# Optimization experiments

Measured on AMD Instinct MI355X. Metric: run time of the kernel, lower is better.

## Reference

```python
import jax, jax.numpy as jnp
import numpy as np

TEMPERATURE = 0.1
TIME_THRESHOLD = 365
NEG = -1e9  # stands in for -inf; exp(NEG - max) == 0 exactly in fp32
EPS = 1e-12  # F.normalize eps


def setup_inputs() -> dict:
    key = jax.random.key(0)
    k1, k2, k3 = jax.random.split(key, 3)
    B, D = 8192, 128
    embeddings = jax.random.normal(k1, (B, D), dtype=jnp.float32)
    survival_times = jax.random.randint(k2, (B,), 0, 3650, dtype=jnp.int32)
    censor = jax.random.randint(k3, (B,), 0, 2, dtype=jnp.int32)
    return {"embeddings": embeddings, "survival_times": survival_times, "censor": censor}


def reference(embeddings, survival_times, censor):
    B = embeddings.shape[0]
    # L2 normalize rows (torch F.normalize semantics)
    norm = jnp.maximum(jnp.linalg.norm(embeddings, axis=1, keepdims=True), EPS)
    z = embeddings / norm
    # pairwise cosine similarity / temperature: [B, B]
    sim = jnp.einsum('ik,jk->ij', z, z) / TEMPERATURE
    diag = jnp.eye(B, dtype=bool)
    sim = jnp.where(diag, NEG, sim)  # mask self-similarity
    # positive mask: |t_i - t_j| < threshold, i != j, row i uncensored
    tdiff = jnp.abs(survival_times[:, None] - survival_times[None, :])
    pos = (tdiff < TIME_THRESHOLD) & (~diag) & (censor[:, None] == 1)
    # per-row masked logsumexp reductions
    denominator = jax.nn.logsumexp(sim, axis=1)                      # [B]
    numerator = jax.nn.logsumexp(jnp.where(pos, sim, NEG), axis=1)   # [B]
    has_pos = jnp.any(pos, axis=1)
    per_row = jnp.where(has_pos, denominator - numerator, 0.0)
    cnt = jnp.sum(has_pos.astype(jnp.float32))
    return jnp.where(cnt > 0, jnp.sum(per_row) / jnp.maximum(cnt, 1.0), 0.0)
```

## Files before the change

kernel.cpp:

```cpp
#include <hip/hip_runtime.h>
#include <cstdint>

#define BDIM 8192
#define DDIM 128
#define JS 32

#define ZH_OFF 0
#define ZL_OFF (2 * 1024 * 1024)
#define RL_OFF (4 * 1024 * 1024)
#define CNT_OFF (RL_OFF + BDIM * 4)
#define FC_OFF (CNT_OFF + 64)
#define P_OFF (RL_OFF + 65536)
#define PART_OFF (P_OFF + BDIM * JS * 8)

typedef __attribute__((ext_vector_type(8))) short bf16x8;
typedef __attribute__((ext_vector_type(4))) float f32x4;

__device__ __forceinline__ short f2bf(float f) {
  unsigned u = __float_as_uint(f);
  unsigned r = (u + 0x7fffu + ((u >> 16) & 1u)) >> 16;
  return (short)r;
}
__device__ __forceinline__ float bf2f(short h) {
  return __uint_as_float(((unsigned)(unsigned short)h) << 16);
}
__device__ __forceinline__ void gload_lds16(const void* g, void* l) {
  __builtin_amdgcn_global_load_lds(
      (const __attribute__((address_space(1))) unsigned int*)g,
      (__attribute__((address_space(3))) unsigned int*)l, 16, 0, 0);
}


__global__ __launch_bounds__(256) void ck_prep(
    const float* __restrict__ emb, const int* __restrict__ censor,
    short* __restrict__ ZhT, short* __restrict__ ZlT,
    int* __restrict__ rowlist, int* __restrict__ cnt, int* __restrict__ fc)
{
  __shared__ float zl[16][132];
  __shared__ float pr[16][16];
  __shared__ float inv[16];
  __shared__ int wtot[4], woff[4];

  const int t = threadIdx.x;
  if (blockIdx.x == 512) {
    const int lane = t & 63, wv = t >> 6;
    const int4* c4 = (const int4*)(censor + t * 32);
    unsigned fm = 0;
#pragma unroll
    for (int q = 0; q < 8; ++q) {
      const int4 v = c4[q];
      fm |= (unsigned)(v.x == 1) << (q * 4 + 0);
      fm |= (unsigned)(v.y == 1) << (q * 4 + 1);
      fm |= (unsigned)(v.z == 1) << (q * 4 + 2);
      fm |= (unsigned)(v.w == 1) << (q * 4 + 3);
    }
    const int loc = __popc(fm);
    int sc = loc;
#pragma unroll
    for (int m = 1; m < 64; m <<= 1) {
      const int u = __shfl_up(sc, m, 64);
      if (lane >= m) sc += u;
    }
    if (lane == 63) wtot[wv] = sc;
    __syncthreads();
    if (t == 0) {
      int run = 0;
#pragma unroll
      for (int i = 0; i < 4; ++i) { woff[i] = run; run += wtot[i]; }
      fc[0] = 0;
    }
    __syncthreads();
    int off = woff[wv] + sc - loc;
    for (int u = 0; u < 32; ++u)
      if ((fm >> u) & 1) rowlist[off++] = t * 32 + u;
    if (t == 255) cnt[0] = off;
    return;
  }

  const int R = blockIdx.x;
  const int r16 = t >> 4, seg = t & 15;
  const float4* src = (const float4*)(emb + (size_t)(R * 16 + r16) * DDIM + seg * 8);
  const float4 v0 = src[0], v1 = src[1];
  float* zr = &zl[r16][seg * 8];
  zr[0] = v0.x; zr[1] = v0.y; zr[2] = v0.z; zr[3] = v0.w;
  zr[4] = v1.x; zr[5] = v1.y; zr[6] = v1.z; zr[7] = v1.w;
  pr[r16][seg] = v0.x * v0.x + v0.y * v0.y + v0.z * v0.z + v0.w * v0.w +
                 v1.x * v1.x + v1.y * v1.y + v1.z * v1.z + v1.w * v1.w;
  __syncthreads();
  if (t < 16) {
    float ss = 0.f;
#pragma unroll
    for (int s = 0; s < 16; ++s) ss += pr[t][s];
    inv[t] = 1.0f / fmaxf(sqrtf(ss), 1e-12f);
  }
  __syncthreads();
  const int kc = t >> 6, hf = (t >> 4) & 3, rw = t & 15;
  const float iv = inv[rw];
  const float* zs = &zl[rw][(kc * 4 + hf) * 8];
  short hs[8], ls[8];
#pragma unroll
  for (int j = 0; j < 8; ++j) {
    const float z = zs[j] * iv;
    const short h = f2bf(z);
    hs[j] = h;
    ls[j] = f2bf(z - bf2f(h));
  }
  const int dst = R * 2048 + t * 8;
  *(bf16x8*)(ZhT + dst) = *(const bf16x8*)hs;
  *(bf16x8*)(ZlT + dst) = *(const bf16x8*)ls;
}

__global__ __launch_bounds__(256, 2) void ck_main(
    const short* __restrict__ ZhT, const short* __restrict__ ZlT,
    const int* __restrict__ rowlist, const int* __restrict__ cntp,
    const int* __restrict__ times, float2* __restrict__ P2)
{
  __shared__ __align__(16) char lds[65536];
  const int cnt = *cntp;
  const int t = threadIdx.x;
  const int b = blockIdx.x;
  const int lane = t & 63;
  const int w = t >> 6;
  const int half = lane >> 4;
  const int ll = lane & 15;
  const int js = b & 31;
  const int jR0 = js * 16;

  for (int g = b >> 5; g * 256 < cnt; g += 16) {
    int rbase[4];
#pragma unroll
    for (int a = 0; a < 4; ++a) {
      int c = g * 256 + w * 64 + a * 16 + ll;
      if (c >= cnt) c = cnt - 1;
      const int r = rowlist[c];
      rbase[a] = (r >> 4) * 2048 + (r & 15) * 8;
    }
    bf16x8 ah[4][4];
#pragma unroll
    for (int a = 0; a < 4; ++a)
#pragma unroll
      for (int kc = 0; kc < 4; ++kc)
        ah[a][kc] = *(const bf16x8*)(ZhT + rbase[a] + kc * 512 + half * 128);

    int meta[4][4];
#pragma unroll
    for (int a = 0; a < 4; ++a)
#pragma unroll
      for (int r = 0; r < 4; ++r) {
        const int idx = g * 256 + w * 64 + a * 16 + half * 4 + r;
        const bool vi = idx < cnt;
        const int gi = rowlist[vi ? idx : 0];
        const int taP = vi ? (times[gi] + 364) : 50000;
        meta[a][r] = (taP << 16) | (vi ? gi : 0xFFFF);
      }

    float sd[4][4] = {{0.f}}, sn[4][4] = {{0.f}};

    {
      const int c0 = w * 8;
#pragma unroll
      for (int u = 0; u < 8; ++u) {
        const int c = c0 + u, cp = c & 15;
        const short* src = (c < 16) ? ZhT : ZlT;
        const short* gp = src + (size_t)(jR0 + (cp >> 2)) * 2048 + (cp & 3) * 512 + lane * 8;
        gload_lds16(gp, lds + ((c < 16) ? 0 : 16384) + cp * 1024);
      }
    }

    for (int st = 0; st < 4; ++st) {
      __syncthreads();
      if (st < 3) {
        const int pB = ((st + 1) & 1) * 32768;
        const int c0 = w * 8;
#pragma unroll
        for (int u = 0; u < 8; ++u) {
          const int c = c0 + u, cp = c & 15;
          const short* src = (c < 16) ? ZhT : ZlT;
          const short* gp = src + (size_t)(jR0 + (st + 1) * 4 + (cp >> 2)) * 2048 + (cp & 3) * 512 + lane * 8;
          gload_lds16(gp, lds + pB + ((c < 16) ? 0 : 16384) + cp * 1024);
        }
      }

      const char* L = lds + (st & 1) * 32768;
      f32x4 acc[4][4];
#pragma unroll
      for (int a = 0; a < 4; ++a)
#pragma unroll
        for (int bb = 0; bb < 4; ++bb) acc[a][bb] = (f32x4){0.f, 0.f, 0.f, 0.f};

#pragma unroll
      for (int kc = 0; kc < 4; ++kc) {
        bf16x8 bh[4], bl[4];
#pragma unroll
        for (int bb = 0; bb < 4; ++bb) {
          bh[bb] = *(const bf16x8*)(L + bb * 4096 + kc * 1024 + lane * 16);
          bl[bb] = *(const bf16x8*)(L + 16384 + bb * 4096 + kc * 1024 + lane * 16);
        }
#pragma unroll
        for (int a = 0; a < 4; ++a)
#pragma unroll
          for (int bb = 0; bb < 4; ++bb)
            acc[a][bb] = __builtin_amdgcn_mfma_f32_16x16x32_bf16(ah[a][kc], bh[bb], acc[a][bb], 0, 0, 0);
#pragma unroll
        for (int a = 0; a < 4; ++a)
#pragma unroll
          for (int bb = 0; bb < 4; ++bb)
            acc[a][bb] = __builtin_amdgcn_mfma_f32_16x16x32_bf16(ah[a][kc], bl[bb], acc[a][bb], 0, 0, 0);
#pragma unroll
        for (int a = 0; a < 4; ++a) {
          const bf16x8 alv = *(const bf16x8*)(ZlT + rbase[a] + kc * 512 + half * 128);
#pragma unroll
          for (int bb = 0; bb < 4; ++bb)
            acc[a][bb] = __builtin_amdgcn_mfma_f32_16x16x32_bf16(alv, bh[bb], acc[a][bb], 0, 0, 0);
        }
      }

      const int jb = js * 256 + st * 64;
      int tJ[4];
#pragma unroll
      for (int bb = 0; bb < 4; ++bb) tJ[bb] = times[jb + bb * 16 + ll];
#pragma unroll
      for (int a = 0; a < 4; ++a)
#pragma unroll
        for (int r = 0; r < 4; ++r) {
          const int m_ = meta[a][r];
          const int gi = m_ & 0xFFFF;
          const unsigned taP = ((unsigned)m_) >> 16;
          float d = 0.f, n = 0.f;
#pragma unroll
          for (int bb = 0; bb < 4; ++bb) {
            const int jgb = jb + bb * 16 + ll;
            float pv = __expf(fmaf(acc[a][bb][r], 10.f, -10.f));
            pv = (gi == jgb) ? 0.f : pv;
            d += pv;
            n += ((unsigned)(taP - (unsigned)tJ[bb]) <= 728u) ? pv : 0.f;
          }
          sd[a][r] += d;
          sn[a][r] += n;
        }
    }

#pragma unroll
    for (int a = 0; a < 4; ++a)
#pragma unroll
      for (int r = 0; r < 4; ++r) {
        float d = sd[a][r], n = sn[a][r];
#pragma unroll
        for (int m = 1; m <= 8; m <<= 1) {
          d += __shfl_xor(d, m, 64);
          n += __shfl_xor(n, m, 64);
        }
        const int idx = g * 256 + w * 64 + a * 16 + half * 4 + r;
        if (ll == 0 && idx < cnt) P2[(size_t)idx * JS + js] = make_float2(d, n);
      }
    __syncthreads();
  }
}

__global__ __launch_bounds__(256) void ck_fin(
    const float2* __restrict__ P2, const int* __restrict__ cntp,
    float2* __restrict__ part, int* __restrict__ fc, float* __restrict__ out)
{
  const int cnt = *cntp;
  const int t = threadIdx.x;
  const int idx = blockIdx.x * 256 + t;
  float lsum = 0.f, lcnt = 0.f;
  if (idx < cnt) {
    const float4* p = (const float4*)(P2 + (size_t)idx * JS);
    float d = 0.f, n = 0.f;
#pragma unroll
    for (int u = 0; u < 16; ++u) {
      const float4 v = p[u];
      d += v.x + v.z;
      n += v.y + v.w;
    }
    if (n > 0.f) { lsum = logf(d) - logf(n); lcnt = 1.f; }
  }
  __shared__ float s1[256], s2[256];
  __shared__ int amLast;
  s1[t] = lsum; s2[t] = lcnt;
  __syncthreads();
  for (int s = 128; s > 0; s >>= 1) {
    if (t < s) { s1[t] += s1[t + s]; s2[t] += s2[t + s]; }
    __syncthreads();
  }
  if (t == 0) {
    part[blockIdx.x] = make_float2(s1[0], s2[0]);
    __threadfence();
    amLast = (atomicAdd(fc, 1) == gridDim.x - 1);
  }
  __syncthreads();
  if (amLast) {
    __threadfence();
    float s = 0.f, c = 0.f;
    if (t < 32) { const float2 v = part[t]; s = v.x; c = v.y; }
    if (t < 64) {
#pragma unroll
      for (int m = 1; m < 64; m <<= 1) {
        s += __shfl_xor(s, m, 64);
        c += __shfl_xor(c, m, 64);
      }
      if (t == 0) out[0] = (c > 0.f) ? s / fmaxf(c, 1.f) : 0.f;
    }
  }
}

extern "C" void kernel_launch(void* const* d_in, const int* in_sizes, int n_in,
                              void* d_out, int out_size, void* d_ws, size_t ws_size,
                              hipStream_t stream) {
  const float* emb  = (const float*)d_in[0];
  const int* times  = (const int*)d_in[1];
  const int* censor = (const int*)d_in[2];
  float* out = (float*)d_out;

  char* ws = (char*)d_ws;
  short* ZhT    = (short*)(ws + ZH_OFF);
  short* ZlT    = (short*)(ws + ZL_OFF);
  int* rowlist  = (int*)(ws + RL_OFF);
  int* cntp     = (int*)(ws + CNT_OFF);
  int* fc       = (int*)(ws + FC_OFF);
  float2* P2    = (float2*)(ws + P_OFF);
  float2* part  = (float2*)(ws + PART_OFF);

  ck_prep<<<513, 256, 0, stream>>>(emb, censor, ZhT, ZlT, rowlist, cntp, fc);
  ck_main<<<512, 256, 0, stream>>>(ZhT, ZlT, rowlist, cntp, times, P2);
  ck_fin<<<32, 256, 0, stream>>>(P2, cntp, part, fc, out);
}
```

Baseline: 131.9 us.

## Replace persistent row-group loop with one 128-row tile per block

The main kernel no longer loops over 256-row groups inside 512 persistent blocks. It now launches 2048 blocks, each handling one 128-row tile (two 16-row subtiles per wave) and exiting early when past the uncensored row count. The MFMA loop is reordered so each B fragment is loaded from LDS once and used immediately for the hi/lo products, which cuts register pressure from 16 accumulators to 8. This aims for better occupancy and load balance. The cost is that each block reloads the full column strip into LDS for fewer rows, so each column tile is reused less.

```diff
diff --git a/kernel.cpp b/kernel.cpp
--- a/kernel.cpp
+++ b/kernel.cpp
@@ -119,142 +119,133 @@
   const int cnt = *cntp;
   const int t = threadIdx.x;
   const int b = blockIdx.x;
+  const int it = b >> 5;
+  const int js = b & 31;
+  if (it * 128 >= cnt) return;
   const int lane = t & 63;
   const int w = t >> 6;
   const int half = lane >> 4;
   const int ll = lane & 15;
-  const int js = b & 31;
   const int jR0 = js * 16;
 
-  for (int g = b >> 5; g * 256 < cnt; g += 16) {
-    int rbase[4];
-#pragma unroll
-    for (int a = 0; a < 4; ++a) {
-      int c = g * 256 + w * 64 + a * 16 + ll;
-      if (c >= cnt) c = cnt - 1;
-      const int r = rowlist[c];
-      rbase[a] = (r >> 4) * 2048 + (r & 15) * 8;
-    }
-    bf16x8 ah[4][4];
-#pragma unroll
-    for (int a = 0; a < 4; ++a)
-#pragma unroll
-      for (int kc = 0; kc < 4; ++kc)
-        ah[a][kc] = *(const bf16x8*)(ZhT + rbase[a] + kc * 512 + half * 128);
-
-    int meta[4][4];
-#pragma unroll
-    for (int a = 0; a < 4; ++a)
-#pragma unroll
-      for (int r = 0; r < 4; ++r) {
-        const int idx = g * 256 + w * 64 + a * 16 + half * 4 + r;
-        const bool vi = idx < cnt;
-        const int gi = rowlist[vi ? idx : 0];
-        const int taP = vi ? (times[gi] + 364) : 50000;
-        meta[a][r] = (taP << 16) | (vi ? gi : 0xFFFF);
-      }
-
-    float sd[4][4] = {{0.f}}, sn[4][4] = {{0.f}};
-
-    {
+  int rbase[2];
+#pragma unroll
+  for (int a = 0; a < 2; ++a) {
+    int c = it * 128 + w * 32 + a * 16 + ll;
+    if (c >= cnt) c = cnt - 1;
+    const int r = rowlist[c];
+    rbase[a] = (r >> 4) * 2048 + (r & 15) * 8;
+  }
+  bf16x8 ah[2][4];
+#pragma unroll
+  for (int a = 0; a < 2; ++a)
+#pragma unroll
+    for (int kc = 0; kc < 4; ++kc)
+      ah[a][kc] = *(const bf16x8*)(ZhT + rbase[a] + kc * 512 + half * 128);
+
+  int meta[2][4];
+#pragma unroll
+  for (int a = 0; a < 2; ++a)
+#pragma unroll
+    for (int r = 0; r < 4; ++r) {
+      const int idx = it * 128 + w * 32 + a * 16 + half * 4 + r;
+      const bool vi = idx < cnt;
+      const int gi = rowlist[vi ? idx : 0];
+      const int taP = vi ? (times[gi] + 364) : 50000;
+      meta[a][r] = (taP << 16) | (vi ? gi : 0xFFFF);
+    }
+
+  float sd[2][4] = {{0.f}}, sn[2][4] = {{0.f}};
+
+  {
+    const int c0 = w * 8;
+#pragma unroll
+    for (int u = 0; u < 8; ++u) {
+      const int c = c0 + u, cp = c & 15;
+      const short* src = (c < 16) ? ZhT : ZlT;
+      const short* gp = src + (size_t)(jR0 + (cp >> 2)) * 2048 + (cp & 3) * 512 + lane * 8;
+      gload_lds16(gp, lds + ((c < 16) ? 0 : 16384) + cp * 1024);
+    }
+  }
+
+  for (int st = 0; st < 4; ++st) {
+    __syncthreads();
+    if (st < 3) {
+      const int pB = ((st + 1) & 1) * 32768;
       const int c0 = w * 8;
 #pragma unroll
       for (int u = 0; u < 8; ++u) {
         const int c = c0 + u, cp = c & 15;
         const short* src = (c < 16) ? ZhT : ZlT;
-        const short* gp = src + (size_t)(jR0 + (cp >> 2)) * 2048 + (cp & 3) * 512 + lane * 8;
-        gload_lds16(gp, lds + ((c < 16) ? 0 : 16384) + cp * 1024);
-      }
-    }
-
-    for (int st = 0; st < 4; ++st) {
-      __syncthreads();
-      if (st < 3) {
-        const int pB = ((st + 1) & 1) * 32768;
-        const int c0 = w * 8;
-#pragma unroll
-        for (int u = 0; u < 8; ++u) {
-          const int c = c0 + u, cp = c & 15;
-          const short* src = (c < 16) ? ZhT : ZlT;
-          const short* gp = src + (size_t)(jR0 + (st + 1) * 4 + (cp >> 2)) * 2048 + (cp & 3) * 512 + lane * 8;
-          gload_lds16(gp, lds + pB + ((c < 16) ? 0 : 16384) + cp * 1024);
+        const short* gp = src + (size_t)(jR0 + (st + 1) * 4 + (cp >> 2)) * 2048 + (cp & 3) * 512 + lane * 8;
+        gload_lds16(gp, lds + pB + ((c < 16) ? 0 : 16384) + cp * 1024);
+      }
+    }
+
+    const char* L = lds + (st & 1) * 32768;
+    f32x4 acc[2][4];
+#pragma unroll
+    for (int a = 0; a < 2; ++a)
+#pragma unroll
+      for (int bb = 0; bb < 4; ++bb) acc[a][bb] = (f32x4){0.f, 0.f, 0.f, 0.f};
+
+#pragma unroll
+    for (int kc = 0; kc < 4; ++kc) {
+      bf16x8 alv[2];
+#pragma unroll
+      for (int a = 0; a < 2; ++a)
+        alv[a] = *(const bf16x8*)(ZlT + rbase[a] + kc * 512 + half * 128);
+#pragma unroll
+      for (int bb = 0; bb < 4; ++bb) {
+        const bf16x8 bhv = *(const bf16x8*)(L + bb * 4096 + kc * 1024 + lane * 16);
+        const bf16x8 blv = *(const bf16x8*)(L + 16384 + bb * 4096 + kc * 1024 + lane * 16);
+        acc[0][bb] = __builtin_amdgcn_mfma_f32_16x16x32_bf16(ah[0][kc], bhv, acc[0][bb], 0, 0, 0);
+        acc[1][bb] = __builtin_amdgcn_mfma_f32_16x16x32_bf16(ah[1][kc], bhv, acc[1][bb], 0, 0, 0);
+        acc[0][bb] = __builtin_amdgcn_mfma_f32_16x16x32_bf16(ah[0][kc], blv, acc[0][bb], 0, 0, 0);
+        acc[1][bb] = __builtin_amdgcn_mfma_f32_16x16x32_bf16(ah[1][kc], blv, acc[1][bb], 0, 0, 0);
+        acc[0][bb] = __builtin_amdgcn_mfma_f32_16x16x32_bf16(alv[0], bhv, acc[0][bb], 0, 0, 0);
+        acc[1][bb] = __builtin_amdgcn_mfma_f32_16x16x32_bf16(alv[1], bhv, acc[1][bb], 0, 0, 0);
+      }
+    }
+
+    const int jb = js * 256 + st * 64;
+    int tJ[4];
+#pragma unroll
+    for (int bb = 0; bb < 4; ++bb) tJ[bb] = times[jb + bb * 16 + ll];
+#pragma unroll
+    for (int a = 0; a < 2; ++a)
+#pragma unroll
+      for (int r = 0; r < 4; ++r) {
+        const int m_ = meta[a][r];
+        const int gi = m_ & 0xFFFF;
+        const unsigned taP = ((unsigned)m_) >> 16;
+        float d = 0.f, n = 0.f;
+#pragma unroll
+        for (int bb = 0; bb < 4; ++bb) {
+          const int jgb = jb + bb * 16 + ll;
+          float pv = __expf(fmaf(acc[a][bb][r], 10.f, -10.f));
+          pv = (gi == jgb) ? 0.f : pv;
+          d += pv;
+          n += ((unsigned)(taP - (unsigned)tJ[bb]) <= 728u) ? pv : 0.f;
         }
-      }
-
-      const char* L = lds + (st & 1) * 32768;
-      f32x4 acc[4][4];
-#pragma unroll
-      for (int a = 0; a < 4; ++a)
-#pragma unroll
-        for (int bb = 0; bb < 4; ++bb) acc[a][bb] = (f32x4){0.f, 0.f, 0.f, 0.f};
-
-#pragma unroll
-      for (int kc = 0; kc < 4; ++kc) {
-        bf16x8 bh[4], bl[4];
-#pragma unroll
-        for (int bb = 0; bb < 4; ++bb) {
-          bh[bb] = *(const bf16x8*)(L + bb * 4096 + kc * 1024 + lane * 16);
-          bl[bb] = *(const bf16x8*)(L + 16384 + bb * 4096 + kc * 1024 + lane * 16);
-        }
-#pragma unroll
-        for (int a = 0; a < 4; ++a)
-#pragma unroll
-          for (int bb = 0; bb < 4; ++bb)
-            acc[a][bb] = __builtin_amdgcn_mfma_f32_16x16x32_bf16(ah[a][kc], bh[bb], acc[a][bb], 0, 0, 0);
-#pragma unroll
-        for (int a = 0; a < 4; ++a)
-#pragma unroll
-          for (int bb = 0; bb < 4; ++bb)
-            acc[a][bb] = __builtin_amdgcn_mfma_f32_16x16x32_bf16(ah[a][kc], bl[bb], acc[a][bb], 0, 0, 0);
-#pragma unroll
-        for (int a = 0; a < 4; ++a) {
-          const bf16x8 alv = *(const bf16x8*)(ZlT + rbase[a] + kc * 512 + half * 128);
-#pragma unroll
-          for (int bb = 0; bb < 4; ++bb)
-            acc[a][bb] = __builtin_amdgcn_mfma_f32_16x16x32_bf16(alv, bh[bb], acc[a][bb], 0, 0, 0);
-        }
-      }
-
-      const int jb = js * 256 + st * 64;
-      int tJ[4];
-#pragma unroll
-      for (int bb = 0; bb < 4; ++bb) tJ[bb] = times[jb + bb * 16 + ll];
-#pragma unroll
-      for (int a = 0; a < 4; ++a)
-#pragma unroll
-        for (int r = 0; r < 4; ++r) {
-          const int m_ = meta[a][r];
-          const int gi = m_ & 0xFFFF;
-          const unsigned taP = ((unsigned)m_) >> 16;
-          float d = 0.f, n = 0.f;
-#pragma unroll
-          for (int bb = 0; bb < 4; ++bb) {
-            const int jgb = jb + bb * 16 + ll;
-            float pv = __expf(fmaf(acc[a][bb][r], 10.f, -10.f));
-            pv = (gi == jgb) ? 0.f : pv;
-            d += pv;
-            n += ((unsigned)(taP - (unsigned)tJ[bb]) <= 728u) ? pv : 0.f;
-          }
-          sd[a][r] += d;
-          sn[a][r] += n;
-        }
-    }
-
-#pragma unroll
-    for (int a = 0; a < 4; ++a)
-#pragma unroll
-      for (int r = 0; r < 4; ++r) {
-        float d = sd[a][r], n = sn[a][r];
-#pragma unroll
-        for (int m = 1; m <= 8; m <<= 1) {
-          d += __shfl_xor(d, m, 64);
-          n += __shfl_xor(n, m, 64);
-        }
-        const int idx = g * 256 + w * 64 + a * 16 + half * 4 + r;
-        if (ll == 0 && idx < cnt) P2[(size_t)idx * JS + js] = make_float2(d, n);
-      }
-    __syncthreads();
-  }
+        sd[a][r] += d;
+        sn[a][r] += n;
+      }
+  }
+
+#pragma unroll
+  for (int a = 0; a < 2; ++a)
+#pragma unroll
+    for (int r = 0; r < 4; ++r) {
+      float d = sd[a][r], n = sn[a][r];
+#pragma unroll
+      for (int m = 1; m <= 8; m <<= 1) {
+        d += __shfl_xor(d, m, 64);
+        n += __shfl_xor(n, m, 64);
+      }
+      const int idx = it * 128 + w * 32 + a * 16 + half * 4 + r;
+      if (ll == 0 && idx < cnt) P2[(size_t)idx * JS + js] = make_float2(d, n);
+    }
 }
 
 __global__ __launch_bounds__(256) void ck_fin(
@@ -323,6 +314,6 @@
   float2* part  = (float2*)(ws + PART_OFF);
 
   ck_prep<<<513, 256, 0, stream>>>(emb, censor, ZhT, ZlT, rowlist, cntp, fc);
-  ck_main<<<512, 256, 0, stream>>>(ZhT, ZlT, rowlist, cntp, times, P2);
+  ck_main<<<64 * 32, 256, 0, stream>>>(ZhT, ZlT, rowlist, cntp, times, P2);
   ck_fin<<<32, 256, 0, stream>>>(P2, cntp, part, fc, out);
 }
```

Measured after the change: 111.0 us. 15.8% less time.

## Use two-term bf16 split with merged mid term and one tile per block

Applied to the files above, without the earlier changes.

The precision split is changed from hi/lo (three MFMA products per k-chunk) to hi plus a 'mid' term m = bf16(2z - h), so that h·m + m·h approximates 2·z·z and the logit is scaled by 5 instead of 10. This removes one third of the MFMA work and the extra lo loads. The main kernel also drops the grid-stride loop in favour of a 1024-block grid with one row tile per block and early exit, and removes the occupancy hint from the launch bounds. The precision loss from dropping the cross-lo terms could shift results slightly.

```diff
diff --git a/kernel.cpp b/kernel.cpp
--- a/kernel.cpp
+++ b/kernel.cpp
@@ -6,7 +6,7 @@
 #define JS 32
 
 #define ZH_OFF 0
-#define ZL_OFF (2 * 1024 * 1024)
+#define ZM_OFF (2 * 1024 * 1024)
 #define RL_OFF (4 * 1024 * 1024)
 #define CNT_OFF (RL_OFF + BDIM * 4)
 #define FC_OFF (CNT_OFF + 64)
@@ -33,7 +33,7 @@
 
 __global__ __launch_bounds__(256) void ck_prep(
     const float* __restrict__ emb, const int* __restrict__ censor,
-    short* __restrict__ ZhT, short* __restrict__ ZlT,
+    short* __restrict__ ZhT, short* __restrict__ ZmT,
     int* __restrict__ rowlist, int* __restrict__ cnt, int* __restrict__ fc)
 {
   __shared__ float zl[16][132];
@@ -97,21 +97,21 @@
   const int kc = t >> 6, hf = (t >> 4) & 3, rw = t & 15;
   const float iv = inv[rw];
   const float* zs = &zl[rw][(kc * 4 + hf) * 8];
-  short hs[8], ls[8];
+  short hs[8], ms[8];
 #pragma unroll
   for (int j = 0; j < 8; ++j) {
     const float z = zs[j] * iv;
     const short h = f2bf(z);
     hs[j] = h;
-    ls[j] = f2bf(z - bf2f(h));
+    ms[j] = f2bf(2.f * z - bf2f(h));
   }
   const int dst = R * 2048 + t * 8;
   *(bf16x8*)(ZhT + dst) = *(const bf16x8*)hs;
-  *(bf16x8*)(ZlT + dst) = *(const bf16x8*)ls;
-}
-
-__global__ __launch_bounds__(256, 2) void ck_main(
-    const short* __restrict__ ZhT, const short* __restrict__ ZlT,
+  *(bf16x8*)(ZmT + dst) = *(const bf16x8*)ms;
+}
+
+__global__ __launch_bounds__(256) void ck_main(
+    const short* __restrict__ ZhT, const short* __restrict__ ZmT,
     const int* __restrict__ rowlist, const int* __restrict__ cntp,
     const int* __restrict__ times, float2* __restrict__ P2)
 {
@@ -119,142 +119,138 @@
   const int cnt = *cntp;
   const int t = threadIdx.x;
   const int b = blockIdx.x;
+  const int it = b >> 5;
+  const int js = b & 31;
+  if (it * 256 >= cnt) return;
   const int lane = t & 63;
   const int w = t >> 6;
   const int half = lane >> 4;
   const int ll = lane & 15;
-  const int js = b & 31;
   const int jR0 = js * 16;
-
-  for (int g = b >> 5; g * 256 < cnt; g += 16) {
-    int rbase[4];
-#pragma unroll
-    for (int a = 0; a < 4; ++a) {
-      int c = g * 256 + w * 64 + a * 16 + ll;
-      if (c >= cnt) c = cnt - 1;
-      const int r = rowlist[c];
-      rbase[a] = (r >> 4) * 2048 + (r & 15) * 8;
-    }
-    bf16x8 ah[4][4];
-#pragma unroll
-    for (int a = 0; a < 4; ++a)
-#pragma unroll
-      for (int kc = 0; kc < 4; ++kc)
-        ah[a][kc] = *(const bf16x8*)(ZhT + rbase[a] + kc * 512 + half * 128);
-
-    int meta[4][4];
-#pragma unroll
-    for (int a = 0; a < 4; ++a)
-#pragma unroll
-      for (int r = 0; r < 4; ++r) {
-        const int idx = g * 256 + w * 64 + a * 16 + half * 4 + r;
-        const bool vi = idx < cnt;
-        const int gi = rowlist[vi ? idx : 0];
-        const int taP = vi ? (times[gi] + 364) : 50000;
-        meta[a][r] = (taP << 16) | (vi ? gi : 0xFFFF);
-      }
-
-    float sd[4][4] = {{0.f}}, sn[4][4] = {{0.f}};
-
-    {
+  const int ibase = it * 256 + w * 64;
+
+  int rbase[4];
+#pragma unroll
+  for (int a = 0; a < 4; ++a) {
+    int c = ibase + a * 16 + ll;
+    if (c >= cnt) c = cnt - 1;
+    const int r = rowlist[c];
+    rbase[a] = (r >> 4) * 2048 + (r & 15) * 8;
+  }
+  bf16x8 ah[4][4];
+#pragma unroll
+  for (int a = 0; a < 4; ++a)
+#pragma unroll
+    for (int kc = 0; kc < 4; ++kc)
+      ah[a][kc] = *(const bf16x8*)(ZhT + rbase[a] + kc * 512 + half * 128);
+
+  int meta[4][4];
+#pragma unroll
+  for (int a = 0; a < 4; ++a)
+#pragma unroll
+    for (int r = 0; r < 4; ++r) {
+      const int idx = ibase + a * 16 + half * 4 + r;
+      const bool vi = idx < cnt;
+      const int gi = rowlist[vi ? idx : 0];
+      const int taP = vi ? (times[gi] + 364) : 50000;
+      meta[a][r] = (taP << 16) | (vi ? gi : 0xFFFF);
+    }
+
+  float sd[4][4] = {{0.f}}, sn[4][4] = {{0.f}};
+
+  {
+    const int c0 = w * 8;
+#pragma unroll
+    for (int u = 0; u < 8; ++u) {
+      const int c = c0 + u, cp = c & 15;
+      const short* src = (c < 16) ? ZhT : ZmT;
+      const short* gp = src + (size_t)(jR0 + (cp >> 2)) * 2048 + (cp & 3) * 512 + lane * 8;
+      gload_lds16(gp, lds + ((c < 16) ? 0 : 16384) + cp * 1024);
+    }
+  }
+
+  for (int st = 0; st < 4; ++st) {
+    __syncthreads();
+    if (st < 3) {
+      const int pB = ((st + 1) & 1) * 32768;
       const int c0 = w * 8;
 #pragma unroll
       for (int u = 0; u < 8; ++u) {
         const int c = c0 + u, cp = c & 15;
-        const short* src = (c < 16) ? ZhT : ZlT;
-        const short* gp = src + (size_t)(jR0 + (cp >> 2)) * 2048 + (cp & 3) * 512 + lane * 8;
-        gload_lds16(gp, lds + ((c < 16) ? 0 : 16384) + cp * 1024);
-      }
-    }
-
-    for (int st = 0; st < 4; ++st) {
-      __syncthreads();
-      if (st < 3) {
-        const int pB = ((st + 1) & 1) * 32768;
-        const int c0 = w * 8;
-#pragma unroll
-        for (int u = 0; u < 8; ++u) {
-          const int c = c0 + u, cp = c & 15;
-          const short* src = (c < 16) ? ZhT : ZlT;
-          const short* gp = src + (size_t)(jR0 + (st + 1) * 4 + (cp >> 2)) * 2048 + (cp & 3) * 512 + lane * 8;
-          gload_lds16(gp, lds + pB + ((c < 16) ? 0 : 16384) + cp * 1024);
+        const short* src = (c < 16) ? ZhT : ZmT;
+        const short* gp = src + (size_t)(jR0 + (st + 1) * 4 + (cp >> 2)) * 2048 + (cp & 3) * 512 + lane * 8;
+        gload_lds16(gp, lds + pB + ((c < 16) ? 0 : 16384) + cp * 1024);
+      }
+    }
+
+    const char* L = lds + (st & 1) * 32768;
+    f32x4 acc[4][4];
+#pragma unroll
+    for (int a = 0; a < 4; ++a)
+#pragma unroll
+      for (int bb = 0; bb < 4; ++bb) acc[a][bb] = (f32x4){0.f, 0.f, 0.f, 0.f};
+
+#pragma unroll
+    for (int kc = 0; kc < 4; ++kc) {
+      bf16x8 bh[4], bm[4], amv[4];
+#pragma unroll
+      for (int bb = 0; bb < 4; ++bb) {
+        bh[bb] = *(const bf16x8*)(L + bb * 4096 + kc * 1024 + lane * 16);
+        bm[bb] = *(const bf16x8*)(L + 16384 + bb * 4096 + kc * 1024 + lane * 16);
+      }
+#pragma unroll
+      for (int a = 0; a < 4; ++a)
+        amv[a] = *(const bf16x8*)(ZmT + rbase[a] + kc * 512 + half * 128);
+#pragma unroll
+      for (int a = 0; a < 4; ++a)
+#pragma unroll
+        for (int bb = 0; bb < 4; ++bb)
+          acc[a][bb] = __builtin_amdgcn_mfma_f32_16x16x32_bf16(ah[a][kc], bm[bb], acc[a][bb], 0, 0, 0);
+#pragma unroll
+      for (int a = 0; a < 4; ++a)
+#pragma unroll
+        for (int bb = 0; bb < 4; ++bb)
+          acc[a][bb] = __builtin_amdgcn_mfma_f32_16x16x32_bf16(amv[a], bh[bb], acc[a][bb], 0, 0, 0);
+    }
+
+    const int jb = js * 256 + st * 64;
+    int tJ[4];
+#pragma unroll
+    for (int bb = 0; bb < 4; ++bb) tJ[bb] = times[jb + bb * 16 + ll];
+#pragma unroll
+    for (int a = 0; a < 4; ++a)
+#pragma unroll
+      for (int r = 0; r < 4; ++r) {
+        const int m_ = meta[a][r];
+        const int gi = m_ & 0xFFFF;
+        const unsigned taP = ((unsigned)m_) >> 16;
+        float d = 0.f, n = 0.f;
+#pragma unroll
+        for (int bb = 0; bb < 4; ++bb) {
+          const int jgb = jb + bb * 16 + ll;
+          float pv = __expf(fmaf(acc[a][bb][r], 5.f, -10.f));
+          pv = (gi == jgb) ? 0.f : pv;
+          d += pv;
+          n += ((unsigned)(taP - (unsigned)tJ[bb]) <= 728u) ? pv : 0.f;
         }
-      }
-
-      const char* L = lds + (st & 1) * 32768;
-      f32x4 acc[4][4];
-#pragma unroll
-      for (int a = 0; a < 4; ++a)
-#pragma unroll
-        for (int bb = 0; bb < 4; ++bb) acc[a][bb] = (f32x4){0.f, 0.f, 0.f, 0.f};
-
-#pragma unroll
-      for (int kc = 0; kc < 4; ++kc) {
-        bf16x8 bh[4], bl[4];
-#pragma unroll
-        for (int bb = 0; bb < 4; ++bb) {
-          bh[bb] = *(const bf16x8*)(L + bb * 4096 + kc * 1024 + lane * 16);
-          bl[bb] = *(const bf16x8*)(L + 16384 + bb * 4096 + kc * 1024 + lane * 16);
-        }
-#pragma unroll
-        for (int a = 0; a < 4; ++a)
-#pragma unroll
-          for (int bb = 0; bb < 4; ++bb)
-            acc[a][bb] = __builtin_amdgcn_mfma_f32_16x16x32_bf16(ah[a][kc], bh[bb], acc[a][bb], 0, 0, 0);
-#pragma unroll
-        for (int a = 0; a < 4; ++a)
-#pragma unroll
-          for (int bb = 0; bb < 4; ++bb)
-            acc[a][bb] = __builtin_amdgcn_mfma_f32_16x16x32_bf16(ah[a][kc], bl[bb], acc[a][bb], 0, 0, 0);
-#pragma unroll
-        for (int a = 0; a < 4; ++a) {
-          const bf16x8 alv = *(const bf16x8*)(ZlT + rbase[a] + kc * 512 + half * 128);
-#pragma unroll
-          for (int bb = 0; bb < 4; ++bb)
-            acc[a][bb] = __builtin_amdgcn_mfma_f32_16x16x32_bf16(alv, bh[bb], acc[a][bb], 0, 0, 0);
-        }
-      }
-
-      const int jb = js * 256 + st * 64;
-      int tJ[4];
-#pragma unroll
-      for (int bb = 0; bb < 4; ++bb) tJ[bb] = times[jb + bb * 16 + ll];
-#pragma unroll
-      for (int a = 0; a < 4; ++a)
-#pragma unroll
-        for (int r = 0; r < 4; ++r) {
-          const int m_ = meta[a][r];
-          const int gi = m_ & 0xFFFF;
-          const unsigned taP = ((unsigned)m_) >> 16;
-          float d = 0.f, n = 0.f;
-#pragma unroll
-          for (int bb = 0; bb < 4; ++bb) {
-            const int jgb = jb + bb * 16 + ll;
-            float pv = __expf(fmaf(acc[a][bb][r], 10.f, -10.f));
-            pv = (gi == jgb) ? 0.f : pv;
-            d += pv;
-            n += ((unsigned)(taP - (unsigned)tJ[bb]) <= 728u) ? pv : 0.f;
-          }
-          sd[a][r] += d;
-          sn[a][r] += n;
-        }
-    }
-
-#pragma unroll
-    for (int a = 0; a < 4; ++a)
-#pragma unroll
-      for (int r = 0; r < 4; ++r) {
-        float d = sd[a][r], n = sn[a][r];
-#pragma unroll
-        for (int m = 1; m <= 8; m <<= 1) {
-          d += __shfl_xor(d, m, 64);
-          n += __shfl_xor(n, m, 64);
-        }
-        const int idx = g * 256 + w * 64 + a * 16 + half * 4 + r;
-        if (ll == 0 && idx < cnt) P2[(size_t)idx * JS + js] = make_float2(d, n);
-      }
-    __syncthreads();
-  }
+        sd[a][r] += d;
+        sn[a][r] += n;
+      }
+  }
+
+#pragma unroll
+  for (int a = 0; a < 4; ++a)
+#pragma unroll
+    for (int r = 0; r < 4; ++r) {
+      float d = sd[a][r], n = sn[a][r];
+#pragma unroll
+      for (int m = 1; m <= 8; m <<= 1) {
+        d += __shfl_xor(d, m, 64);
+        n += __shfl_xor(n, m, 64);
+      }
+      const int idx = ibase + a * 16 + half * 4 + r;
+      if (ll == 0 && idx < cnt) P2[(size_t)idx * JS + js] = make_float2(d, n);
+    }
 }
 
 __global__ __launch_bounds__(256) void ck_fin(
@@ -287,7 +283,7 @@
   if (t == 0) {
     part[blockIdx.x] = make_float2(s1[0], s2[0]);
     __threadfence();
-    amLast = (atomicAdd(fc, 1) == gridDim.x - 1);
+    amLast = (atomicAdd(fc, 1) == (int)gridDim.x - 1);
   }
   __syncthreads();
   if (amLast) {
@@ -315,14 +311,14 @@
 
   char* ws = (char*)d_ws;
   short* ZhT    = (short*)(ws + ZH_OFF);
-  short* ZlT    = (short*)(ws + ZL_OFF);
+  short* ZmT    = (short*)(ws + ZM_OFF);
   int* rowlist  = (int*)(ws + RL_OFF);
   int* cntp     = (int*)(ws + CNT_OFF);
   int* fc       = (int*)(ws + FC_OFF);
   float2* P2    = (float2*)(ws + P_OFF);
   float2* part  = (float2*)(ws + PART_OFF);
 
-  ck_prep<<<513, 256, 0, stream>>>(emb, censor, ZhT, ZlT, rowlist, cntp, fc);
-  ck_main<<<512, 256, 0, stream>>>(ZhT, ZlT, rowlist, cntp, times, P2);
+  ck_prep<<<513, 256, 0, stream>>>(emb, censor, ZhT, ZmT, rowlist, cntp, fc);
+  ck_main<<<32 * 32, 256, 0, stream>>>(ZhT, ZmT, rowlist, cntp, times, P2);
   ck_fin<<<32, 256, 0, stream>>>(P2, cntp, part, fc, out);
 }
```

Measured after the change: 117.1 us. 11.2% less time.
